# Optimization experiments

Hardware: AMD Instinct MI355X
Metric: run time of the kernel (lower is better)

The kernel has to match this reference:

```python
import jax, jax.numpy as jnp
import numpy as np
from jax import lax

# Fixed image shape (H, W) for all images, standard detection resize
H_IMG, W_IMG = 800.0, 1333.0
SCORE_THRESH = 0.05
NMS_THRESH = 0.5
DET_PER_IMG = 100
K_PRE = 2048  # NMS candidate budget per image (after score threshold)
BBOX_XFORM_CLIP = float(np.log(1000.0 / 16.0))
WX, WY, WW, WH = 10.0, 10.0, 5.0, 5.0  # bbox_reg_weights


def setup_inputs() -> dict:
    B, P, C = 8, 2000, 81
    key = jax.random.key(0)
    k1, k2, k3, k4 = jax.random.split(key, 4)
    class_logits = 2.0 * jax.random.normal(k1, (B * P, C), jnp.float32)
    box_regression = 0.5 * jax.random.normal(k2, (B * P, C * 4), jnp.float32)
    # valid proposal boxes inside the image: (x1,y1) + (w,h)
    xy = jax.random.uniform(k3, (B, P, 2), jnp.float32) * jnp.array([W_IMG - 128.0, H_IMG - 128.0], jnp.float32)
    wh = 1.0 + 127.0 * jax.random.uniform(k4, (B, P, 2), jnp.float32)
    proposals = jnp.concatenate([xy, xy + wh], axis=-1)
    return {"class_logits": class_logits, "box_regression": box_regression, "proposals": proposals}


def _decode(rel, boxes):
    # BoxCoder.decode: rel [N, C, 4], boxes [N, 4] -> [N, C, 4]
    w = boxes[:, 2] - boxes[:, 0]
    h = boxes[:, 3] - boxes[:, 1]
    cx = boxes[:, 0] + 0.5 * w
    cy = boxes[:, 1] + 0.5 * h
    dx = rel[..., 0] / WX
    dy = rel[..., 1] / WY
    dw = jnp.minimum(rel[..., 2] / WW, BBOX_XFORM_CLIP)
    dh = jnp.minimum(rel[..., 3] / WH, BBOX_XFORM_CLIP)
    pcx = dx * w[:, None] + cx[:, None]
    pcy = dy * h[:, None] + cy[:, None]
    pw = jnp.exp(dw) * w[:, None]
    ph = jnp.exp(dh) * h[:, None]
    return jnp.stack([pcx - 0.5 * pw, pcy - 0.5 * ph, pcx + 0.5 * pw, pcy + 0.5 * ph], axis=-1)


def _pairwise_iou(b):
    # b: [K, 4] -> [K, K]
    area = jnp.maximum(b[:, 2] - b[:, 0], 0.0) * jnp.maximum(b[:, 3] - b[:, 1], 0.0)
    lt = jnp.maximum(b[:, None, :2], b[None, :, :2])
    rb = jnp.minimum(b[:, None, 2:], b[None, :, 2:])
    wh = jnp.maximum(rb - lt, 0.0)
    inter = wh[..., 0] * wh[..., 1]
    union = area[:, None] + area[None, :] - inter
    return inter / jnp.maximum(union, 1e-9)


def _greedy_nms(boxes, valid):
    # boxes: [K, 4] sorted by score desc; valid: [K] bool. Exact greedy NMS.
    K = boxes.shape[0]
    iou = _pairwise_iou(boxes)
    idx = jnp.arange(K)

    def body(i, keep):
        sup = keep[i] & (iou[i] > NMS_THRESH) & (idx > i)
        return keep & ~sup

    return lax.fori_loop(0, K, body, valid)


def reference(class_logits, box_regression, proposals):
    B, P, _ = proposals.shape
    C = class_logits.shape[-1]
    # decode all class-specific boxes, softmax scores
    rel = box_regression.reshape(-1, C, 4)
    pred = _decode(rel, proposals.reshape(-1, 4)).reshape(B, P, C, 4)
    scores = jax.nn.softmax(class_logits, axis=-1).reshape(B, P, C)
    # drop background class 0
    M = P * (C - 1)
    boxes = pred[:, :, 1:, :].reshape(B, M, 4)
    scores = scores[:, :, 1:].reshape(B, M)
    labels = jnp.broadcast_to(jnp.arange(1, C)[None, None, :], (B, P, C - 1)).reshape(B, M)
    # clip to image
    x1 = jnp.clip(boxes[..., 0], 0.0, W_IMG)
    y1 = jnp.clip(boxes[..., 1], 0.0, H_IMG)
    x2 = jnp.clip(boxes[..., 2], 0.0, W_IMG)
    y2 = jnp.clip(boxes[..., 3], 0.0, H_IMG)
    boxes = jnp.stack([x1, y1, x2, y2], axis=-1)
    # score threshold + remove_small_boxes(min_size=0.01), as a validity mask
    valid = (scores > SCORE_THRESH) & ((x2 - x1) >= 0.01) & ((y2 - y1) >= 0.01)
    masked = jnp.where(valid, scores, -1.0)
    # top-K candidates per image (sorted desc -> NMS visiting order)
    top_s, top_i = lax.top_k(masked, K_PRE)
    top_b = jnp.take_along_axis(boxes, top_i[..., None], axis=1)
    top_l = jnp.take_along_axis(labels, top_i, axis=1)
    top_v = top_s > 0.0
    # batched_nms: per-class coordinate offsets so classes never overlap
    off = top_l.astype(jnp.float32) * (jnp.maximum(W_IMG, H_IMG) + 1.0)
    keep = jax.vmap(_greedy_nms)(top_b + off[..., None], top_v)
    final = jnp.where(keep, top_s, -1.0)
    det_s, det_i = lax.top_k(final, DET_PER_IMG)
    det_b = jnp.take_along_axis(top_b, det_i[..., None], axis=1)
    det_l = jnp.take_along_axis(top_l, det_i, axis=1)
    det_valid = det_s > 0.0  # padding slots have score -1
    return det_b, det_s, det_l, det_valid
```

## Files before the change

### kernel.cpp

```cpp
#include <hip/hip_runtime.h>
#include <cstdint>
#include <cstddef>

typedef unsigned long long u64;

constexpr int Bn   = 8;
constexpr int Pn   = 2000;
constexpr int Cn   = 81;
constexpr int CM1  = 80;
constexpr int KPRE = 2048;
constexpr int NDET = 100;
constexpr int SECP = 8;
constexpr int NSEC2 = Pn / SECP;
constexpr int SSLOT = 160;
constexpr int CAP  = 4096;
constexpr int NBINS = 5632;
constexpr int BINOFF = (122 << 10);
constexpr float W_IMG = 1333.0f;
constexpr float H_IMG = 800.0f;
constexpr float XFORM_CLIP = 4.135166556742356f;
constexpr float NMS_OFF = 1334.0f;

constexpr size_t OFF_SL = 0;
constexpr size_t OFF_SC = (size_t)Bn * NSEC2 * SSLOT * 8;

__device__ __forceinline__ void decode_clip(const float4 rv, float w, float h,
                                            float cx, float cy, float out[4]) {
  float dx = rv.x / 10.0f;
  float dy = rv.y / 10.0f;
  float dw = fminf(rv.z / 5.0f, XFORM_CLIP);
  float dh = fminf(rv.w / 5.0f, XFORM_CLIP);
  float pcx = dx * w + cx;
  float pcy = dy * h + cy;
  float pw = expf(dw) * w;
  float ph = expf(dh) * h;
  out[0] = fminf(fmaxf(pcx - 0.5f * pw, 0.0f), W_IMG);
  out[1] = fminf(fmaxf(pcy - 0.5f * ph, 0.0f), H_IMG);
  out[2] = fminf(fmaxf(pcx + 0.5f * pw, 0.0f), W_IMG);
  out[3] = fminf(fmaxf(pcy + 0.5f * ph, 0.0f), H_IMG);
}

__device__ __forceinline__ int score_bin(unsigned bits) {
  int bin = (int)(bits >> 13) - BINOFF;
  return min(max(bin, 0), NBINS - 1);
}

__device__ __forceinline__ void key_decode(u64 key, int b,
                                           const float* __restrict__ reg,
                                           const float* __restrict__ props,
                                           float bx[4], int& label, float& sc) {
  sc = __uint_as_float((unsigned)(key >> 32));
  bx[0] = bx[1] = bx[2] = bx[3] = 0.0f;
  label = 0;
  if (key != 0ull) {
    int m = (int)(0xFFFFFFFFu - (unsigned)key);
    int p = m / CM1;
    int c = m - p * CM1 + 1;
    int nidx = b * Pn + p;
    const float4 pb = *reinterpret_cast<const float4*>(props + (size_t)nidx * 4);
    float w = pb.z - pb.x, h = pb.w - pb.y;
    float cx = pb.x + 0.5f * w, cy = pb.y + 0.5f * h;
    float4 rv = *reinterpret_cast<const float4*>(reg + (size_t)nidx * (Cn * 4) + c * 4);
    decode_clip(rv, w, h, cx, cy, bx);
    label = c;
  }
}

__global__ __launch_bounds__(256) void
k1_score(const float* __restrict__ logits, const float* __restrict__ reg,
         const float* __restrict__ props, u64* __restrict__ slices,
         int* __restrict__ scnt) {
  int blk = blockIdx.x, t = threadIdx.x, lane = t & 63, wv = t >> 6;
  int b = blk / NSEC2, sec = blk % NSEC2;
  __shared__ u64 cbuf[SSLOT];
  __shared__ int cnt_sh;
  if (t == 0) cnt_sh = 0;
  __syncthreads();

  #pragma unroll
  for (int pp = wv; pp < SECP; pp += 4) {
    int p = sec * SECP + pp;
    int wid = b * Pn + p;
    const float* lg = logits + (size_t)wid * Cn;
    float x0 = lg[lane];
    float x1 = (lane < Cn - 64) ? lg[64 + lane] : -3.4e38f;
    float mx = fmaxf(x0, x1);
    for (int m = 32; m; m >>= 1) mx = fmaxf(mx, __shfl_xor(mx, m, 64));
    float e0 = expf(x0 - mx);
    float e1 = (lane < Cn - 64) ? expf(x1 - mx) : 0.0f;
    float ssum = e0 + e1;
    for (int m = 32; m; m >>= 1) ssum += __shfl_xor(ssum, m, 64);

    const float4 pb = *reinterpret_cast<const float4*>(props + (size_t)wid * 4);
    float w = pb.z - pb.x, h = pb.w - pb.y;
    float cx = pb.x + 0.5f * w, cy = pb.y + 0.5f * h;
    const float* rrow = reg + (size_t)wid * (Cn * 4);

    u64 key0 = 0ull, key1 = 0ull;
    if (lane >= 1) {
      float sc = e0 / ssum;
      if (sc > 0.05f) {
        float4 rv = *reinterpret_cast<const float4*>(rrow + lane * 4);
        float bx[4];
        decode_clip(rv, w, h, cx, cy, bx);
        if ((bx[2] - bx[0] >= 0.01f) && (bx[3] - bx[1] >= 0.01f)) {
          unsigned m = (unsigned)(p * CM1 + (lane - 1));
          key0 = ((u64)__float_as_uint(sc) << 32) | (0xFFFFFFFFu - m);
        }
      }
    }
    if (lane < Cn - 64) {
      int c = 64 + lane;
      float sc = e1 / ssum;
      if (sc > 0.05f) {
        float4 rv = *reinterpret_cast<const float4*>(rrow + c * 4);
        float bx[4];
        decode_clip(rv, w, h, cx, cy, bx);
        if ((bx[2] - bx[0] >= 0.01f) && (bx[3] - bx[1] >= 0.01f)) {
          unsigned m = (unsigned)(p * CM1 + (c - 1));
          key1 = ((u64)__float_as_uint(sc) << 32) | (0xFFFFFFFFu - m);
        }
      }
    }
    u64 bal0 = __ballot(key0 != 0ull);
    u64 bal1 = __ballot(key1 != 0ull);
    int tot = __popcll(bal0) + __popcll(bal1);
    if (tot) {
      int base = 0;
      if (lane == 0) base = atomicAdd(&cnt_sh, tot);
      base = __shfl(base, 0, 64);
      int r0 = __popcll(bal0 & ((1ull << lane) - 1ull));
      int r1 = __popcll(bal0) + __popcll(bal1 & ((1ull << lane) - 1ull));
      if (key0) cbuf[base + r0] = key0;
      if (key1) cbuf[base + r1] = key1;
    }
  }
  __syncthreads();
  int n = cnt_sh;
  for (int i = t; i < n; i += 256) slices[(size_t)blk * SSLOT + i] = cbuf[i];
  if (t == 0) scnt[blk] = n;
}

template <int CHV>
__device__ __forceinline__ void mp_round(u64* buf, int base, int nA, int nB,
                                         int outLen, int tid) {
  const u64* A = buf + base;
  const u64* B = buf + base + nA;
  int d = tid * CHV;
  u64 rg[CHV];
  int cnt = 0;
  if (d < outLen) {
    int lo = max(0, d - nB), hi = min(d, nA);
    while (lo < hi) {
      int mid = (lo + hi) >> 1;
      if (A[mid] >= B[d - 1 - mid]) lo = mid + 1; else hi = mid;
    }
    int i = lo, j = d - lo;
    for (int e = 0; e < CHV && d + e < outLen; e++) {
      u64 v;
      if (j >= nB || (i < nA && A[i] >= B[j])) v = A[i++];
      else v = B[j++];
      rg[cnt++] = v;
    }
  }
  __syncthreads();
  for (int e = 0; e < cnt; e++) buf[base + d + e] = rg[e];
  __syncthreads();
}

template <int CHV>
__device__ __forceinline__ void mp_seg_round(u64* buf, int len, int cnt, int t) {
  int tps = len / CHV;
  int seg = t / tps;
  int tid = t - seg * tps;
  int base = seg * len;
  bool act = (base < cnt);
  int nA = len >> 1;
  int d = tid * CHV;
  u64 rg[CHV];
  if (act) {
    const u64* A = buf + base;
    const u64* B = buf + base + nA;
    int lo = max(0, d - nA), hi = min(d, nA);
    while (lo < hi) {
      int mid = (lo + hi) >> 1;
      if (A[mid] >= B[d - 1 - mid]) lo = mid + 1; else hi = mid;
    }
    int i = lo, j = d - lo;
    #pragma unroll
    for (int e = 0; e < CHV; e++) {
      u64 v;
      if (j >= nA || (i < nA && A[i] >= B[j])) v = A[i++];
      else v = B[j++];
      rg[e] = v;
    }
  }
  __syncthreads();
  if (act) {
    #pragma unroll
    for (int e = 0; e < CHV; e++) buf[base + d + e] = rg[e];
  }
  __syncthreads();
}

__global__ __launch_bounds__(1024) void
k2_fused(const u64* __restrict__ slices, const int* __restrict__ scnt,
         const float* __restrict__ reg, const float* __restrict__ props,
         float* __restrict__ out) {
  int b = blockIdx.x, t = threadIdx.x, lane = t & 63, w = t >> 6;
  __shared__ u64 bufA[CAP];
  __shared__ u64 keys2[KPRE];
  __shared__ u64 maskb[256][4];
  __shared__ u64 keepw[KPRE / 64];
  __shared__ int accI[NDET];
  __shared__ int hlds[NBINS];
  __shared__ int lcnt[NSEC2];
  __shared__ int sufAfter[256];
  __shared__ int chunkTot[4];
  __shared__ int tmax_sh, cnt_sh, kcnt_sh;
  float4* obox = (float4*)bufA;

  for (int i = t; i < NBINS; i += 1024) hlds[i] = 0;
  for (int i = t; i < CAP; i += 1024) bufA[i] = 0ull;
  if (t < NSEC2) lcnt[t] = scnt[b * NSEC2 + t];
  if (t == 0) { tmax_sh = 0; cnt_sh = 0; }
  __syncthreads();

  for (int sec = w; sec < NSEC2; sec += 16) {
    int n = lcnt[sec];
    const u64* sl = slices + (size_t)(b * NSEC2 + sec) * SSLOT;
    for (int i0 = 0; i0 < n; i0 += 64) {
      int i = i0 + lane;
      u64 key = (i < n) ? sl[i] : 0ull;
      bool has = key != 0ull;
      u64 bal = __ballot(has);
      int tot = __popcll(bal);
      if (tot) {
        int base = 0;
        if (lane == 0) base = atomicAdd(&cnt_sh, tot);
        base = __shfl(base, 0, 64);
        int rank = __popcll(bal & ((1ull << lane) - 1ull));
        int pos = base + rank;
        if (has) {
          if (pos < CAP) bufA[pos] = key;
          atomicAdd(&hlds[score_bin((unsigned)(key >> 32))], 1);
        }
      }
    }
  }
  __syncthreads();
  int rawcnt = cnt_sh;
  int cnt;
  if (rawcnt <= CAP) {
    cnt = rawcnt;
  } else {
    const int CH = NBINS / 256;
    int suf = 0;
    if (t < 256) {
      int lo = t * CH;
      int s = 0;
      #pragma unroll
      for (int i = 0; i < CH; i++) s += hlds[lo + i];
      for (int d2 = 1; d2 < 64; d2 <<= 1) {
        int v = __shfl_down(s, d2, 64);
        if (lane + d2 < 64) s += v;
      }
      if (lane == 0) chunkTot[t >> 6] = s;
      suf = s;
    }
    __syncthreads();
    if (t < 256) {
      int w4 = t >> 6;
      for (int q = w4 + 1; q < 4; q++) suf += chunkTot[q];
      sufAfter[t] = suf;
    }
    __syncthreads();
    if (t < 256) {
      int lo = t * CH, hi = lo + CH;
      int cum = (t + 1 < 256) ? sufAfter[t + 1] : 0;
      int cand = -1;
      for (int i = hi - 1; i >= lo; i--) {
        cum += hlds[i];
        if (cum >= KPRE) { cand = i; break; }
      }
      if (cand >= 0) atomicMax(&tmax_sh, cand);
    }
    __syncthreads();
    int T = tmax_sh;
    for (int i = t; i < CAP; i += 1024) bufA[i] = 0ull;
    if (t == 0) cnt_sh = 0;
    __syncthreads();
    for (int sec = w; sec < NSEC2; sec += 16) {
      int n = lcnt[sec];
      const u64* sl = slices + (size_t)(b * NSEC2 + sec) * SSLOT;
      for (int i0 = 0; i0 < n; i0 += 64) {
        int i = i0 + lane;
        u64 key = (i < n) ? sl[i] : 0ull;
        bool pass = key && (score_bin((unsigned)(key >> 32)) >= T);
        u64 bal = __ballot(pass);
        int tot = __popcll(bal);
        if (tot) {
          int base = 0;
          if (lane == 0) base = atomicAdd(&cnt_sh, tot);
          base = __shfl(base, 0, 64);
          int rank = __popcll(bal & ((1ull << lane) - 1ull));
          int pos = base + rank;
          if (pass && pos < CAP) bufA[pos] = key;
        }
      }
    }
    __syncthreads();
    cnt = min(cnt_sh, CAP);
  }

  for (int r = w; (r << 6) < cnt; r += 16) {
    u64 v = bufA[(r << 6) | lane];
    #pragma unroll
    for (int k = 2; k <= 64; k <<= 1) {
      #pragma unroll
      for (int j = k >> 1; j > 0; j >>= 1) {
        u64 o = __shfl_xor(v, j, 64);
        bool dir = ((lane & k) == 0);
        bool lower = ((lane & j) == 0);
        u64 mn = (v < o) ? v : o;
        u64 mx = (v < o) ? o : v;
        v = (dir == lower) ? mx : mn;
      }
    }
    bufA[(r << 6) | lane] = v;
  }
  __syncthreads();

  mp_seg_round<4>(bufA, 128, cnt, t);
  mp_seg_round<4>(bufA, 256, cnt, t);
  mp_seg_round<4>(bufA, 512, cnt, t);
  mp_seg_round<4>(bufA, 1024, cnt, t);
  mp_seg_round<4>(bufA, 2048, cnt, t);
  if (cnt > 2048)
    mp_round<2>(bufA, 0, 2048, 2048, 2048, t);

  u64 k0 = bufA[t], k1v = bufA[t + 1024];
  keys2[t] = k0;
  keys2[t + 1024] = k1v;
  {
    u64 bal = __ballot(k0 != 0ull);
    if (lane == 0) keepw[w] = bal;
    bal = __ballot(k1v != 0ull);
    if (lane == 0) keepw[16 + w] = bal;
  }
  __syncthreads();
  #pragma unroll
  for (int s = 0; s < 2; s++) {
    int j = t + s * 1024;
    u64 key = s ? k1v : k0;
    float bx[4]; int label; float sc;
    key_decode(key, b, reg, props, bx, label, sc);
    float off = (float)label * NMS_OFF;
    obox[j] = make_float4(bx[0] + off, bx[1] + off, bx[2] + off, bx[3] + off);
  }
  __syncthreads();

  int kcount = 0;
  for (int w0 = 0; w0 < KPRE && kcount < NDET; w0 += 256) {
    if (w0 > 0 && kcount > 0) {
      if (t < 256) {
        int j = w0 + t;
        u64 kwv = keepw[j >> 6];
        bool alive = (kwv >> (j & 63)) & 1ull;
        if (alive) {
          float4 jb = obox[j];
          float jar = fmaxf(jb.z - jb.x, 0.0f) * fmaxf(jb.w - jb.y, 0.0f);
          for (int a = 0; a < kcount; a++) {
            float4 ab = obox[accI[a]];
            float ix1 = fmaxf(ab.x, jb.x), iy1 = fmaxf(ab.y, jb.y);
            float ix2 = fminf(ab.z, jb.z), iy2 = fminf(ab.w, jb.w);
            float iw = fmaxf(ix2 - ix1, 0.0f), ih = fmaxf(iy2 - iy1, 0.0f);
            float inter = iw * ih;
            if (inter > 0.0f) {
              float aar = fmaxf(ab.z - ab.x, 0.0f) * fmaxf(ab.w - ab.y, 0.0f);
              float iou = inter / fmaxf(aar + jar - inter, 1e-9f);
              if (iou > 0.5f) { alive = false; break; }
            }
          }
        }
        u64 bal = __ballot(alive);
        if (lane == 0) keepw[(w0 >> 6) + (t >> 6)] = bal;
      }
      __syncthreads();
    }
    {
      int r = t >> 2, wd = t & 3;
      int rgp = w0 + r;
      bool ralive = (keepw[rgp >> 6] >> (rgp & 63)) & 1ull;
      float4 rb = obox[rgp];
      float rar = fmaxf(rb.z - rb.x, 0.0f) * fmaxf(rb.w - rb.y, 0.0f);
      u64 m = 0;
      if (ralive) {
        int cb0 = w0 + wd * 64;
        for (int jj = 0; jj < 64; jj++) {
          int cg = cb0 + jj;
          float4 cb = obox[cg];
          float ix1 = fmaxf(rb.x, cb.x), iy1 = fmaxf(rb.y, cb.y);
          float ix2 = fminf(rb.z, cb.z), iy2 = fminf(rb.w, cb.w);
          float iw = fmaxf(ix2 - ix1, 0.0f), ih = fmaxf(iy2 - iy1, 0.0f);
          float inter = iw * ih;
          if (inter > 0.0f && cg > rgp) {
            float car = fmaxf(cb.z - cb.x, 0.0f) * fmaxf(cb.w - cb.y, 0.0f);
            float iou = inter / fmaxf(rar + car - inter, 1e-9f);
            if (iou > 0.5f) m |= (1ull << jj);
          }
        }
      }
      maskb[r][wd] = m;
    }
    __syncthreads();
    if (w == 0) {
      u64 kw0 = keepw[(w0 >> 6) + 0];
      u64 kw1 = keepw[(w0 >> 6) + 1];
      u64 kw2 = keepw[(w0 >> 6) + 2];
      u64 kw3 = keepw[(w0 >> 6) + 3];
      int kc = kcount;
      #pragma unroll
      for (int wq = 0; wq < 4; wq++) {
        u64 cw = (wq == 0) ? kw0 : (wq == 1) ? kw1 : (wq == 2) ? kw2 : kw3;
        if (cw == 0ull) continue;
        for (int rb0 = 0; rb0 < 64 && kc < NDET; rb0 += 4) {
          u64 gbits = (cw >> rb0) & 0xFull;
          int r = wq * 64 + rb0;
          u64 rm0a = maskb[r][0],   rm0b = maskb[r][1],   rm0c = maskb[r][2],   rm0d = maskb[r][3];
          u64 rm1a = maskb[r+1][0], rm1b = maskb[r+1][1], rm1c = maskb[r+1][2], rm1d = maskb[r+1][3];
          u64 rm2a = maskb[r+2][0], rm2b = maskb[r+2][1], rm2c = maskb[r+2][2], rm2d = maskb[r+2][3];
          u64 rm3a = maskb[r+3][0], rm3b = maskb[r+3][1], rm3c = maskb[r+3][2], rm3d = maskb[r+3][3];
          if (gbits == 0ull) continue;
          #pragma unroll
          for (int d = 0; d < 4; d++) {
            u64 cwq = (wq == 0) ? kw0 : (wq == 1) ? kw1 : (wq == 2) ? kw2 : kw3;
            if ((cwq >> (rb0 + d)) & 1ull) {
              if (lane == 0) accI[kc] = w0 + r + d;
              kc++;
              if (kc >= NDET) break;
              u64 ma = (d == 0) ? rm0a : (d == 1) ? rm1a : (d == 2) ? rm2a : rm3a;
              u64 mb = (d == 0) ? rm0b : (d == 1) ? rm1b : (d == 2) ? rm2b : rm3b;
              u64 mc = (d == 0) ? rm0c : (d == 1) ? rm1c : (d == 2) ? rm2c : rm3c;
              u64 md = (d == 0) ? rm0d : (d == 1) ? rm1d : (d == 2) ? rm2d : rm3d;
              kw0 &= ~ma; kw1 &= ~mb; kw2 &= ~mc; kw3 &= ~md;
            }
          }
          cw = (wq == 0) ? kw0 : (wq == 1) ? kw1 : (wq == 2) ? kw2 : kw3;
        }
      }
      if (lane == 0) {
        keepw[(w0 >> 6) + 0] = kw0;
        keepw[(w0 >> 6) + 1] = kw1;
        keepw[(w0 >> 6) + 2] = kw2;
        keepw[(w0 >> 6) + 3] = kw3;
        kcnt_sh = kc;
      }
    }
    __syncthreads();
    kcount = kcnt_sh;
  }

  if (t == 0 && kcount < NDET) {
    int run = kcount;
    for (int wq = 0; wq < KPRE / 64 && run < NDET; wq++) {
      u64 nk = ~keepw[wq];
      while (nk && run < NDET) {
        int bit2 = __ffsll((long long)nk) - 1;
        nk &= nk - 1;
        accI[run++] = wq * 64 + bit2;
      }
    }
  }
  __syncthreads();

  if (t < NDET) {
    int k = accI[t];
    bool kept = t < kcount;
    u64 key = keys2[k];
    float bx[4]; int label; float sc;
    key_decode(key, b, reg, props, bx, label, sc);
    int oi = b * NDET + t;
    out[(size_t)oi * 4 + 0] = bx[0];
    out[(size_t)oi * 4 + 1] = bx[1];
    out[(size_t)oi * 4 + 2] = bx[2];
    out[(size_t)oi * 4 + 3] = bx[3];
    out[Bn * NDET * 4 + oi] = kept ? sc : -1.0f;
    out[Bn * NDET * 5 + oi] = (float)label;
    out[Bn * NDET * 6 + oi] = kept ? 1.0f : 0.0f;
  }
}

extern "C" void kernel_launch(void* const* d_in, const int* in_sizes, int n_in,
                              void* d_out, int out_size, void* d_ws, size_t ws_size,
                              hipStream_t stream) {
  const float* logits = (const float*)d_in[0];
  const float* reg    = (const float*)d_in[1];
  const float* props  = (const float*)d_in[2];
  float* out = (float*)d_out;
  char* ws = (char*)d_ws;

  u64* slices = (u64*)(ws + OFF_SL);
  int* scnt   = (int*)(ws + OFF_SC);

  k1_score<<<Bn * NSEC2, 256, 0, stream>>>(logits, reg, props, slices, scnt);
  k2_fused<<<Bn, 1024, 0, stream>>>(slices, scnt, reg, props, out);
}
```

Baseline: 135.6 us.

## Enlarge candidate buffer to skip histogram pass and prefetch slice loads

Raises the shared candidate buffer capacity so the common case fits without the score-histogram threshold pass. The histogram now reuses the buffer memory and runs only on overflow, which drops the per-key shared atomics from the main gather. The gather loop prefetches the next section's first chunk while appending the current one, and the merge-sort rounds become cnt-gated with more elements per thread and extra levels for larger counts. The cost is a much larger shared-memory footprint (128KB buffer) and deeper sort merges whenever counts exceed 2048.

```diff
diff --git a/kernel.cpp b/kernel.cpp
--- a/kernel.cpp
+++ b/kernel.cpp
@@ -13,7 +13,7 @@
 constexpr int SECP = 8;
 constexpr int NSEC2 = Pn / SECP;
 constexpr int SSLOT = 160;
-constexpr int CAP  = 4096;
+constexpr int CAP  = 16384;
 constexpr int NBINS = 5632;
 constexpr int BINOFF = (122 << 10);
 constexpr float W_IMG = 1333.0f;
@@ -203,6 +203,20 @@
   __syncthreads();
 }
 
+__device__ __forceinline__ void append_chunk(u64 key, bool valid,
+                                             u64* bufA, int* cnt_sh, int lane) {
+  u64 bal = __ballot(valid);
+  int tot = __popcll(bal);
+  if (tot) {
+    int base = 0;
+    if (lane == 0) base = atomicAdd(cnt_sh, tot);
+    base = __shfl(base, 0, 64);
+    int rank = __popcll(bal & ((1ull << lane) - 1ull));
+    int pos = base + rank;
+    if (valid && pos < CAP) bufA[pos] = key;
+  }
+}
+
 __global__ __launch_bounds__(1024) void
 k2_fused(const u64* __restrict__ slices, const int* __restrict__ scnt,
          const float* __restrict__ reg, const float* __restrict__ props,
@@ -213,54 +227,67 @@
   __shared__ u64 maskb[256][4];
   __shared__ u64 keepw[KPRE / 64];
   __shared__ int accI[NDET];
-  __shared__ int hlds[NBINS];
   __shared__ int lcnt[NSEC2];
   __shared__ int sufAfter[256];
   __shared__ int chunkTot[4];
   __shared__ int tmax_sh, cnt_sh, kcnt_sh;
   float4* obox = (float4*)bufA;
 
-  for (int i = t; i < NBINS; i += 1024) hlds[i] = 0;
   for (int i = t; i < CAP; i += 1024) bufA[i] = 0ull;
   if (t < NSEC2) lcnt[t] = scnt[b * NSEC2 + t];
   if (t == 0) { tmax_sh = 0; cnt_sh = 0; }
   __syncthreads();
 
-  for (int sec = w; sec < NSEC2; sec += 16) {
-    int n = lcnt[sec];
-    const u64* sl = slices + (size_t)(b * NSEC2 + sec) * SSLOT;
-    for (int i0 = 0; i0 < n; i0 += 64) {
-      int i = i0 + lane;
-      u64 key = (i < n) ? sl[i] : 0ull;
-      bool has = key != 0ull;
-      u64 bal = __ballot(has);
-      int tot = __popcll(bal);
-      if (tot) {
-        int base = 0;
-        if (lane == 0) base = atomicAdd(&cnt_sh, tot);
-        base = __shfl(base, 0, 64);
-        int rank = __popcll(bal & ((1ull << lane) - 1ull));
-        int pos = base + rank;
-        if (has) {
-          if (pos < CAP) bufA[pos] = key;
-          atomicAdd(&hlds[score_bin((unsigned)(key >> 32))], 1);
+  {
+    int sec = w;
+    int n0 = 0; u64 kv = 0ull;
+    if (sec < NSEC2) {
+      n0 = lcnt[sec];
+      if (lane < n0) kv = slices[(size_t)(b * NSEC2 + sec) * SSLOT + lane];
+    }
+    while (sec < NSEC2) {
+      int nsec = sec + 16;
+      int n1 = 0; u64 kn = 0ull;
+      if (nsec < NSEC2) {
+        n1 = lcnt[nsec];
+        if (lane < n1)
+          kn = slices[(size_t)(b * NSEC2 + nsec) * SSLOT + lane];
+      }
+      append_chunk(kv, lane < n0 && kv != 0ull, bufA, &cnt_sh, lane);
+      for (int i0 = 64; i0 < n0; i0 += 64) {
+        int i = i0 + lane;
+        u64 ke = (i < n0) ? slices[(size_t)(b * NSEC2 + sec) * SSLOT + i] : 0ull;
+        append_chunk(ke, ke != 0ull, bufA, &cnt_sh, lane);
+      }
+      sec = nsec; n0 = n1; kv = kn;
+    }
+  }
+  __syncthreads();
+  int cnt = cnt_sh;
+
+  if (cnt > CAP) {
+    int* hl = (int*)bufA;
+    for (int i = t; i < NBINS; i += 1024) hl[i] = 0;
+    __syncthreads();
+    for (int sec = w; sec < NSEC2; sec += 16) {
+      int n = lcnt[sec];
+      const u64* sl = slices + (size_t)(b * NSEC2 + sec) * SSLOT;
+      for (int i0 = 0; i0 < n; i0 += 64) {
+        int i = i0 + lane;
+        if (i < n) {
+          u64 key = sl[i];
+          if (key) atomicAdd(&hl[score_bin((unsigned)(key >> 32))], 1);
         }
       }
     }
-  }
-  __syncthreads();
-  int rawcnt = cnt_sh;
-  int cnt;
-  if (rawcnt <= CAP) {
-    cnt = rawcnt;
-  } else {
+    __syncthreads();
     const int CH = NBINS / 256;
     int suf = 0;
     if (t < 256) {
       int lo = t * CH;
       int s = 0;
       #pragma unroll
-      for (int i = 0; i < CH; i++) s += hlds[lo + i];
+      for (int i = 0; i < CH; i++) s += hl[lo + i];
       for (int d2 = 1; d2 < 64; d2 <<= 1) {
         int v = __shfl_down(s, d2, 64);
         if (lane + d2 < 64) s += v;
@@ -280,7 +307,7 @@
       int cum = (t + 1 < 256) ? sufAfter[t + 1] : 0;
       int cand = -1;
       for (int i = hi - 1; i >= lo; i--) {
-        cum += hlds[i];
+        cum += hl[i];
         if (cum >= KPRE) { cand = i; break; }
       }
       if (cand >= 0) atomicMax(&tmax_sh, cand);
@@ -297,16 +324,7 @@
         int i = i0 + lane;
         u64 key = (i < n) ? sl[i] : 0ull;
         bool pass = key && (score_bin((unsigned)(key >> 32)) >= T);
-        u64 bal = __ballot(pass);
-        int tot = __popcll(bal);
-        if (tot) {
-          int base = 0;
-          if (lane == 0) base = atomicAdd(&cnt_sh, tot);
-          base = __shfl(base, 0, 64);
-          int rank = __popcll(bal & ((1ull << lane) - 1ull));
-          int pos = base + rank;
-          if (pass && pos < CAP) bufA[pos] = key;
-        }
+        append_chunk(key, pass, bufA, &cnt_sh, lane);
       }
     }
     __syncthreads();
@@ -331,13 +349,14 @@
   }
   __syncthreads();
 
-  mp_seg_round<4>(bufA, 128, cnt, t);
-  mp_seg_round<4>(bufA, 256, cnt, t);
-  mp_seg_round<4>(bufA, 512, cnt, t);
-  mp_seg_round<4>(bufA, 1024, cnt, t);
-  mp_seg_round<4>(bufA, 2048, cnt, t);
-  if (cnt > 2048)
-    mp_round<2>(bufA, 0, 2048, 2048, 2048, t);
+  if (cnt > 64)   mp_seg_round<16>(bufA, 128, cnt, t);
+  if (cnt > 128)  mp_seg_round<16>(bufA, 256, cnt, t);
+  if (cnt > 256)  mp_seg_round<16>(bufA, 512, cnt, t);
+  if (cnt > 512)  mp_seg_round<16>(bufA, 1024, cnt, t);
+  if (cnt > 1024) mp_seg_round<16>(bufA, 2048, cnt, t);
+  if (cnt > 2048) mp_seg_round<16>(bufA, 4096, cnt, t);
+  if (cnt > 4096) mp_seg_round<16>(bufA, 8192, cnt, t);
+  if (cnt > 8192) mp_round<2>(bufA, 0, 8192, 8192, 2048, t);
 
   u64 k0 = bufA[t], k1v = bufA[t + 1024];
   keys2[t] = k0;
```

Result: slower. 175.5 us (+29.4%).

## Split per-image sort into four segment-sort blocks plus merge-and-NMS kernel

Applied to the files above, without the earlier changes.

Replaces the single per-image fused kernel, which gathered all candidates, ran a histogram threshold pass and sorted everything in one block, with two kernels. Four blocks per image each gather and sort a quarter of the sections into a top-2048 run. A final per-image block merges the four runs and does NMS. The histogram-based threshold fallback is removed because each segment keeps its own top-2048. k1 also moves to 512 threads so each wave handles one proposal, and the gather prefetches the next slice. This spreads the sort across 32 blocks instead of 8, at the cost of an extra launch and a global round trip for the runs.

```diff
diff --git a/kernel.cpp b/kernel.cpp
--- a/kernel.cpp
+++ b/kernel.cpp
@@ -13,16 +13,17 @@
 constexpr int SECP = 8;
 constexpr int NSEC2 = Pn / SECP;
 constexpr int SSLOT = 160;
-constexpr int CAP  = 4096;
-constexpr int NBINS = 5632;
-constexpr int BINOFF = (122 << 10);
+constexpr int NSEG = 4;
+constexpr int RUNL = 2048;
+constexpr int K2CAP = 4096;
 constexpr float W_IMG = 1333.0f;
 constexpr float H_IMG = 800.0f;
 constexpr float XFORM_CLIP = 4.135166556742356f;
 constexpr float NMS_OFF = 1334.0f;
 
-constexpr size_t OFF_SL = 0;
-constexpr size_t OFF_SC = (size_t)Bn * NSEC2 * SSLOT * 8;
+constexpr size_t OFF_SL   = 0;
+constexpr size_t OFF_SC   = (size_t)Bn * NSEC2 * SSLOT * 8;
+constexpr size_t OFF_RUNS = OFF_SC + (size_t)Bn * NSEC2 * 4;
 
 __device__ __forceinline__ void decode_clip(const float4 rv, float w, float h,
                                             float cx, float cy, float out[4]) {
@@ -38,11 +39,6 @@
   out[1] = fminf(fmaxf(pcy - 0.5f * ph, 0.0f), H_IMG);
   out[2] = fminf(fmaxf(pcx + 0.5f * pw, 0.0f), W_IMG);
   out[3] = fminf(fmaxf(pcy + 0.5f * ph, 0.0f), H_IMG);
-}
-
-__device__ __forceinline__ int score_bin(unsigned bits) {
-  int bin = (int)(bits >> 13) - BINOFF;
-  return min(max(bin, 0), NBINS - 1);
 }
 
 __device__ __forceinline__ void key_decode(u64 key, int b,
@@ -66,7 +62,7 @@
   }
 }
 
-__global__ __launch_bounds__(256) void
+__global__ __launch_bounds__(512) void
 k1_score(const float* __restrict__ logits, const float* __restrict__ reg,
          const float* __restrict__ props, u64* __restrict__ slices,
          int* __restrict__ scnt) {
@@ -77,9 +73,8 @@
   if (t == 0) cnt_sh = 0;
   __syncthreads();
 
-  #pragma unroll
-  for (int pp = wv; pp < SECP; pp += 4) {
-    int p = sec * SECP + pp;
+  {
+    int p = sec * SECP + wv;
     int wid = b * Pn + p;
     const float* lg = logits + (size_t)wid * Cn;
     float x0 = lg[lane];
@@ -137,7 +132,7 @@
   }
   __syncthreads();
   int n = cnt_sh;
-  for (int i = t; i < n; i += 256) slices[(size_t)blk * SSLOT + i] = cbuf[i];
+  for (int i = t; i < n; i += 512) slices[(size_t)blk * SSLOT + i] = cbuf[i];
   if (t == 0) scnt[blk] = n;
 }
 
@@ -203,118 +198,66 @@
   __syncthreads();
 }
 
+__device__ __forceinline__ void append_chunk(u64 key, bool valid, u64* buf,
+                                             int* cnt_sh, int lane) {
+  u64 bal = __ballot(valid);
+  int tot = __popcll(bal);
+  if (tot) {
+    int base = 0;
+    if (lane == 0) base = atomicAdd(cnt_sh, tot);
+    base = __shfl(base, 0, 64);
+    int rank = __popcll(bal & ((1ull << lane) - 1ull));
+    int pos = base + rank;
+    if (valid && pos < K2CAP) buf[pos] = key;
+  }
+}
+
 __global__ __launch_bounds__(1024) void
-k2_fused(const u64* __restrict__ slices, const int* __restrict__ scnt,
-         const float* __restrict__ reg, const float* __restrict__ props,
-         float* __restrict__ out) {
-  int b = blockIdx.x, t = threadIdx.x, lane = t & 63, w = t >> 6;
-  __shared__ u64 bufA[CAP];
-  __shared__ u64 keys2[KPRE];
-  __shared__ u64 maskb[256][4];
-  __shared__ u64 keepw[KPRE / 64];
-  __shared__ int accI[NDET];
-  __shared__ int hlds[NBINS];
-  __shared__ int lcnt[NSEC2];
-  __shared__ int sufAfter[256];
-  __shared__ int chunkTot[4];
-  __shared__ int tmax_sh, cnt_sh, kcnt_sh;
-  float4* obox = (float4*)bufA;
-
-  for (int i = t; i < NBINS; i += 1024) hlds[i] = 0;
-  for (int i = t; i < CAP; i += 1024) bufA[i] = 0ull;
-  if (t < NSEC2) lcnt[t] = scnt[b * NSEC2 + t];
-  if (t == 0) { tmax_sh = 0; cnt_sh = 0; }
-  __syncthreads();
-
-  for (int sec = w; sec < NSEC2; sec += 16) {
-    int n = lcnt[sec];
-    const u64* sl = slices + (size_t)(b * NSEC2 + sec) * SSLOT;
-    for (int i0 = 0; i0 < n; i0 += 64) {
-      int i = i0 + lane;
-      u64 key = (i < n) ? sl[i] : 0ull;
-      bool has = key != 0ull;
-      u64 bal = __ballot(has);
-      int tot = __popcll(bal);
-      if (tot) {
-        int base = 0;
-        if (lane == 0) base = atomicAdd(&cnt_sh, tot);
-        base = __shfl(base, 0, 64);
-        int rank = __popcll(bal & ((1ull << lane) - 1ull));
-        int pos = base + rank;
-        if (has) {
-          if (pos < CAP) bufA[pos] = key;
-          atomicAdd(&hlds[score_bin((unsigned)(key >> 32))], 1);
-        }
-      }
-    }
-  }
-  __syncthreads();
-  int rawcnt = cnt_sh;
-  int cnt;
-  if (rawcnt <= CAP) {
-    cnt = rawcnt;
-  } else {
-    const int CH = NBINS / 256;
-    int suf = 0;
-    if (t < 256) {
-      int lo = t * CH;
-      int s = 0;
-      #pragma unroll
-      for (int i = 0; i < CH; i++) s += hlds[lo + i];
-      for (int d2 = 1; d2 < 64; d2 <<= 1) {
-        int v = __shfl_down(s, d2, 64);
-        if (lane + d2 < 64) s += v;
-      }
-      if (lane == 0) chunkTot[t >> 6] = s;
-      suf = s;
-    }
-    __syncthreads();
-    if (t < 256) {
-      int w4 = t >> 6;
-      for (int q = w4 + 1; q < 4; q++) suf += chunkTot[q];
-      sufAfter[t] = suf;
-    }
-    __syncthreads();
-    if (t < 256) {
-      int lo = t * CH, hi = lo + CH;
-      int cum = (t + 1 < 256) ? sufAfter[t + 1] : 0;
-      int cand = -1;
-      for (int i = hi - 1; i >= lo; i--) {
-        cum += hlds[i];
-        if (cum >= KPRE) { cand = i; break; }
-      }
-      if (cand >= 0) atomicMax(&tmax_sh, cand);
-    }
-    __syncthreads();
-    int T = tmax_sh;
-    for (int i = t; i < CAP; i += 1024) bufA[i] = 0ull;
-    if (t == 0) cnt_sh = 0;
-    __syncthreads();
-    for (int sec = w; sec < NSEC2; sec += 16) {
-      int n = lcnt[sec];
-      const u64* sl = slices + (size_t)(b * NSEC2 + sec) * SSLOT;
-      for (int i0 = 0; i0 < n; i0 += 64) {
+k2b_sort(const u64* __restrict__ slices, const int* __restrict__ scnt,
+         u64* __restrict__ runs) {
+  int blk = blockIdx.x, t = threadIdx.x, lane = t & 63, w = t >> 6;
+  int b = blk >> 2, seg = blk & 3;
+  int s0 = seg * 62 + min(seg, 2);
+  int ns = 62 + (seg < 2 ? 1 : 0);
+  __shared__ u64 buf[K2CAP];
+  __shared__ int lcnt2[63];
+  __shared__ int cnt_sh;
+  if (t == 0) cnt_sh = 0;
+  if (t < ns) lcnt2[t] = scnt[b * NSEC2 + s0 + t];
+  __syncthreads();
+
+  {
+    int sl = w;
+    int n0 = 0; u64 kv = 0ull;
+    if (sl < ns) {
+      n0 = lcnt2[sl];
+      if (lane < n0) kv = slices[(size_t)(b * NSEC2 + s0 + sl) * SSLOT + lane];
+    }
+    while (sl < ns) {
+      int nx = sl + 16;
+      int n1 = 0; u64 kn = 0ull;
+      if (nx < ns) {
+        n1 = lcnt2[nx];
+        if (lane < n1)
+          kn = slices[(size_t)(b * NSEC2 + s0 + nx) * SSLOT + lane];
+      }
+      append_chunk(kv, (lane < n0) && (kv != 0ull), buf, &cnt_sh, lane);
+      for (int i0 = 64; i0 < n0; i0 += 64) {
         int i = i0 + lane;
-        u64 key = (i < n) ? sl[i] : 0ull;
-        bool pass = key && (score_bin((unsigned)(key >> 32)) >= T);
-        u64 bal = __ballot(pass);
-        int tot = __popcll(bal);
-        if (tot) {
-          int base = 0;
-          if (lane == 0) base = atomicAdd(&cnt_sh, tot);
-          base = __shfl(base, 0, 64);
-          int rank = __popcll(bal & ((1ull << lane) - 1ull));
-          int pos = base + rank;
-          if (pass && pos < CAP) bufA[pos] = key;
-        }
-      }
-    }
-    __syncthreads();
-    cnt = min(cnt_sh, CAP);
-  }
+        u64 ke = (i < n0) ? slices[(size_t)(b * NSEC2 + s0 + sl) * SSLOT + i]
+                          : 0ull;
+        append_chunk(ke, ke != 0ull, buf, &cnt_sh, lane);
+      }
+      sl = nx; n0 = n1; kv = kn;
+    }
+  }
+  __syncthreads();
+  int cnt = min(cnt_sh, K2CAP);
+  for (int i = cnt + t; i < K2CAP; i += 1024) buf[i] = 0ull;
+  __syncthreads();
 
   for (int r = w; (r << 6) < cnt; r += 16) {
-    u64 v = bufA[(r << 6) | lane];
+    u64 v = buf[(r << 6) | lane];
     #pragma unroll
     for (int k = 2; k <= 64; k <<= 1) {
       #pragma unroll
@@ -327,21 +270,78 @@
         v = (dir == lower) ? mx : mn;
       }
     }
-    bufA[(r << 6) | lane] = v;
-  }
-  __syncthreads();
-
-  mp_seg_round<4>(bufA, 128, cnt, t);
-  mp_seg_round<4>(bufA, 256, cnt, t);
-  mp_seg_round<4>(bufA, 512, cnt, t);
-  mp_seg_round<4>(bufA, 1024, cnt, t);
-  mp_seg_round<4>(bufA, 2048, cnt, t);
-  if (cnt > 2048)
-    mp_round<2>(bufA, 0, 2048, 2048, 2048, t);
-
-  u64 k0 = bufA[t], k1v = bufA[t + 1024];
-  keys2[t] = k0;
-  keys2[t + 1024] = k1v;
+    buf[(r << 6) | lane] = v;
+  }
+  __syncthreads();
+
+  if (cnt > 64)   mp_seg_round<4>(buf, 128, cnt, t);
+  if (cnt > 128)  mp_seg_round<4>(buf, 256, cnt, t);
+  if (cnt > 256)  mp_seg_round<4>(buf, 512, cnt, t);
+  if (cnt > 512)  mp_seg_round<4>(buf, 1024, cnt, t);
+  if (cnt > 1024) mp_seg_round<4>(buf, 2048, cnt, t);
+  if (cnt > 2048) mp_round<2>(buf, 0, 2048, 2048, 2048, t);
+
+  for (int i = t; i < RUNL; i += 1024)
+    runs[(size_t)blk * RUNL + i] = buf[i];
+}
+
+__global__ __launch_bounds__(1024) void
+k3_nms(const u64* __restrict__ runs, const float* __restrict__ reg,
+       const float* __restrict__ props, float* __restrict__ out) {
+  int b = blockIdx.x, t = threadIdx.x, lane = t & 63, w = t >> 6;
+  __shared__ u64 bufS[NSEG * RUNL];
+  __shared__ u64 bufD[NSEG * RUNL];
+  __shared__ u64 maskb[256][4];
+  __shared__ u64 keepw[KPRE / 64];
+  __shared__ int accI[NDET];
+  __shared__ int kcnt_sh;
+  float4* obox = (float4*)bufD;
+
+  for (int i = t; i < NSEG * RUNL; i += 1024)
+    bufS[i] = runs[(size_t)b * NSEG * RUNL + i];
+  __syncthreads();
+
+  #pragma unroll
+  for (int p = 0; p < 2; p++) {
+    const u64* A = bufS + p * 4096;
+    const u64* B = A + 2048;
+    int d = t * 4;
+    int lo = max(0, d - 2048), hi = min(d, 2048);
+    while (lo < hi) {
+      int mid = (lo + hi) >> 1;
+      if (A[mid] >= B[d - 1 - mid]) lo = mid + 1; else hi = mid;
+    }
+    int i = lo, j = d - lo;
+    #pragma unroll
+    for (int e = 0; e < 4; e++) {
+      u64 v;
+      if (j >= 2048 || (i < 2048 && A[i] >= B[j])) v = A[i++];
+      else v = B[j++];
+      bufD[p * 4096 + d + e] = v;
+    }
+  }
+  __syncthreads();
+  {
+    const u64* A = bufD;
+    const u64* B = bufD + 4096;
+    int d = t * 2;
+    int lo = max(0, d - 4096), hi = min(d, 4096);
+    while (lo < hi) {
+      int mid = (lo + hi) >> 1;
+      if (A[mid] >= B[d - 1 - mid]) lo = mid + 1; else hi = mid;
+    }
+    int i = lo, j = d - lo;
+    #pragma unroll
+    for (int e = 0; e < 2; e++) {
+      u64 v;
+      if (j >= 4096 || (i < 4096 && A[i] >= B[j])) v = A[i++];
+      else v = B[j++];
+      bufS[d + e] = v;
+    }
+  }
+  __syncthreads();
+
+  u64 k0 = bufS[t], k1v = bufS[t + 1024];
   {
     u64 bal = __ballot(k0 != 0ull);
     if (lane == 0) keepw[w] = bal;
@@ -477,7 +477,7 @@
   if (t < NDET) {
     int k = accI[t];
     bool kept = t < kcount;
-    u64 key = keys2[k];
+    u64 key = bufS[k];
     float bx[4]; int label; float sc;
     key_decode(key, b, reg, props, bx, label, sc);
     int oi = b * NDET + t;
@@ -502,7 +502,9 @@
 
   u64* slices = (u64*)(ws + OFF_SL);
   int* scnt   = (int*)(ws + OFF_SC);
-
-  k1_score<<<Bn * NSEC2, 256, 0, stream>>>(logits, reg, props, slices, scnt);
-  k2_fused<<<Bn, 1024, 0, stream>>>(slices, scnt, reg, props, out);
-}
+  u64* runs   = (u64*)(ws + OFF_RUNS);
+
+  k1_score<<<Bn * NSEC2, 512, 0, stream>>>(logits, reg, props, slices, scnt);
+  k2b_sort<<<Bn * NSEG, 1024, 0, stream>>>(slices, scnt, runs);
+  k3_nms<<<Bn, 1024, 0, stream>>>(runs, reg, props, out);
+}
```

New measurement: 127.0 us. 6.3% less time.
